# Kernel optimization log

Hardware: AMD Instinct MI355X
Metric: run time of the kernel (lower is better)

## Reference

```python
import jax, jax.numpy as jnp
import numpy as np

B, C_IN, C_OUT, C_KEY, N = 8, 512, 512, 256, 2048


def setup_inputs() -> dict:
    key = jax.random.key(0)
    k1, k2, k3, k4 = jax.random.split(key, 4)
    x = jax.random.normal(k1, (B, C_IN, N), dtype=jnp.float32)
    # Conv1d(kernel=1, bias=False) weights -> plain linear maps over channel dim
    Wq = jax.random.normal(k2, (C_KEY, C_IN), dtype=jnp.float32) * (1.0 / np.sqrt(C_IN))
    Wk = jax.random.normal(k3, (C_KEY, C_IN), dtype=jnp.float32) * (1.0 / np.sqrt(C_IN))
    Wv = jax.random.normal(k4, (C_OUT, C_IN), dtype=jnp.float32) * (1.0 / np.sqrt(C_IN))
    return {"x": x, "Wq": Wq, "Wk": Wk, "Wv": Wv}


def reference(x, Wq, Wk, Wv):
    # 1x1 conv projections: [B, C, N] -> [B, Ck/Co, N]
    q = jnp.einsum("oc,bcn->bon", Wq, x)
    k = jnp.einsum("oc,bcn->bon", Wk, x)
    v = jnpqv = jnp.einsum("oc,bcn->bon", Wv, x)
    # sim_map[b,i,j] = sum_c k[b,c,i] * q[b,c,j]  (unscaled)
    sim = jnp.einsum("bci,bcj->bij", k, q)  # [B, N, N]
    attn = jax.nn.softmax(sim, axis=-1)
    # out = value @ sim_map, then permute(0,2,1) -> [B, N, C_out]
    out = jnp.einsum("bck,bkm->bmc", jnpqv, attn)
    return out
```

## Files before the change

kernel.cpp:

```cpp
#include <hip/hip_runtime.h>

typedef _Float16 half8 __attribute__((ext_vector_type(8)));
typedef _Float16 half4v __attribute__((ext_vector_type(4)));
typedef _Float16 half2v __attribute__((ext_vector_type(2)));
typedef float f32x4 __attribute__((ext_vector_type(4)));

#define ASYNC_CP16(gp, lp)                                       \
  __builtin_amdgcn_global_load_lds(                              \
      (const __attribute__((address_space(1))) void*)(gp),       \
      (__attribute__((address_space(3))) void*)(lp), 16, 0, 0)

__global__ __launch_bounds__(256) void conv_w(const float* __restrict__ Wq,
                                              const float* __restrict__ Wk,
                                              const float* __restrict__ Wv,
                                              _Float16* __restrict__ Wb) {
  int idx = blockIdx.x * 256 + threadIdx.x;
  int row = idx >> 9;
  float v;
  if (row < 256)      v = Wq[idx];
  else if (row < 512) v = Wk[idx - 256 * 512];
  else                v = Wv[idx - 512 * 512];
  Wb[idx] = (_Float16)v;
}

__global__ __launch_bounds__(256) void conv_xT(const float* __restrict__ x,
                                               _Float16* __restrict__ xT) {
  __shared__ float T[32][33];
  const int b = blockIdx.z;
  const int n0 = blockIdx.x * 32, c0 = blockIdx.y * 32;
  const int t = threadIdx.x;
  const float* xb = x + (size_t)b * 512 * 2048;
  const int n2 = t & 15, cr = t >> 4;
#pragma unroll
  for (int r = 0; r < 2; r++) {
    int c = cr + r * 16;
    float2 v = *(const float2*)&xb[(size_t)(c0 + c) * 2048 + n0 + n2 * 2];
    T[c][n2 * 2] = v.x;
    T[c][n2 * 2 + 1] = v.y;
  }
  __syncthreads();
  _Float16* xtb = xT + (size_t)b * 2048 * 512;
  const int c2 = t & 15, nr = t >> 4;
#pragma unroll
  for (int r = 0; r < 2; r++) {
    int n = nr + r * 16;
    half2v h;
    h[0] = (_Float16)T[c2 * 2][n];
    h[1] = (_Float16)T[c2 * 2 + 1][n];
    *(half2v*)&xtb[(size_t)(n0 + n) * 512 + c0 + c2 * 2] = h;
  }
}

template <typename OutT, bool TR, bool STATS>
__global__ __launch_bounds__(256) void gemm_nt(const _Float16* __restrict__ A,
                                               const _Float16* __restrict__ B,
                                               OutT* __restrict__ C, int K,
                                               int lda, int ldb, int ldc,
                                               long sA, long sB, long sC,
                                               float* __restrict__ pm,
                                               float* __restrict__ ps) {
  A += (size_t)blockIdx.z * sA;
  B += (size_t)blockIdx.z * sB;
  C += (size_t)blockIdx.z * sC;
  const int m_blk = blockIdx.y * 128, n_blk = blockIdx.x * 128;

  __shared__ _Float16 As[2][4096];
  __shared__ _Float16 Bs[2][4096];

  const int t = threadIdx.x;
  const int lane = t & 63, wave = t >> 6;
  const int quad = lane >> 4, l16 = lane & 15;
  const int wm = (wave & 1) * 64, wn = (wave >> 1) * 64;

  const int srow = 16 * wave + (lane >> 2);
  const int schunk = (lane & 3) ^ ((lane >> 3) & 3);
  const _Float16* gA0 = A + (size_t)(m_blk + srow) * lda + schunk * 8;
  const _Float16* gA1 = gA0 + (size_t)64 * lda;
  const _Float16* gB0 = B + (size_t)(n_blk + srow) * ldb + schunk * 8;
  const _Float16* gB1 = gB0 + (size_t)64 * ldb;
  const int lofs = wave * 512 + lane * 8;

  const int rchunk = (quad ^ ((l16 >> 1) & 3)) * 8;

  f32x4 acc[4][4] = {};

  ASYNC_CP16(gA0, &As[0][lofs]);
  ASYNC_CP16(gA1, &As[0][lofs + 2048]);
  ASYNC_CP16(gB0, &Bs[0][lofs]);
  ASYNC_CP16(gB1, &Bs[0][lofs + 2048]);

  int ib = 0;
  for (int k0 = 0; k0 < K; k0 += 32, ib ^= 1) {
    __syncthreads();
    if (k0 + 32 < K) {
      ASYNC_CP16(gA0 + k0 + 32, &As[ib ^ 1][lofs]);
      ASYNC_CP16(gA1 + k0 + 32, &As[ib ^ 1][lofs + 2048]);
      ASYNC_CP16(gB0 + k0 + 32, &Bs[ib ^ 1][lofs]);
      ASYNC_CP16(gB1 + k0 + 32, &Bs[ib ^ 1][lofs + 2048]);
    }
    half8 af[4], bf[4];
#pragma unroll
    for (int i = 0; i < 4; i++) {
      af[i] = *(const half8*)&As[ib][(wm + i * 16 + l16) * 32 + rchunk];
      bf[i] = *(const half8*)&Bs[ib][(wn + i * 16 + l16) * 32 + rchunk];
    }
#pragma unroll
    for (int i = 0; i < 4; i++)
#pragma unroll
      for (int j = 0; j < 4; j++)
        acc[i][j] =
            __builtin_amdgcn_mfma_f32_16x16x32_f16(af[i], bf[j], acc[i][j], 0, 0, 0);
  }

#pragma unroll
  for (int i = 0; i < 4; i++) {
    const int m0 = m_blk + wm + i * 16 + quad * 4;
#pragma unroll
    for (int j = 0; j < 4; j++) {
      const int n0 = n_blk + wn + j * 16 + l16;
      if constexpr (TR) {
        if constexpr (sizeof(OutT) == 4) {
          *(f32x4*)&C[(size_t)n0 * ldc + m0] = acc[i][j];
        } else {
          half4v h;
          h[0] = (_Float16)acc[i][j][0];
          h[1] = (_Float16)acc[i][j][1];
          h[2] = (_Float16)acc[i][j][2];
          h[3] = (_Float16)acc[i][j][3];
          *(half4v*)&C[(size_t)n0 * ldc + m0] = h;
        }
      } else {
#pragma unroll
        for (int r = 0; r < 4; r++)
          C[(size_t)(m0 + r) * ldc + n0] = (OutT)acc[i][j][r];
      }
    }
  }

  if constexpr (STATS) {
    __shared__ float sred[2][128][2];
    const int wng = wave >> 1;
    float bmax[4][4], bsum[4][4];
#pragma unroll
    for (int i = 0; i < 4; i++) {
#pragma unroll
      for (int r = 0; r < 4; r++) {
        float mx = acc[i][0][r];
#pragma unroll
        for (int j = 1; j < 4; j++) mx = fmaxf(mx, acc[i][j][r]);
#pragma unroll
        for (int d = 1; d < 16; d <<= 1)
          mx = fmaxf(mx, __shfl_xor(mx, d, 64));
        float es = 0.f;
#pragma unroll
        for (int j = 0; j < 4; j++) es += __expf(acc[i][j][r] - mx);
#pragma unroll
        for (int d = 1; d < 16; d <<= 1) es += __shfl_xor(es, d, 64);
        bmax[i][r] = mx;
        bsum[i][r] = es;
      }
    }
    if (l16 == 0) {
#pragma unroll
      for (int i = 0; i < 4; i++)
#pragma unroll
        for (int r = 0; r < 4; r++) {
          int ml = wm + i * 16 + quad * 4 + r;
          sred[wng][ml][0] = bmax[i][r];
          sred[wng][ml][1] = bsum[i][r];
        }
    }
    __syncthreads();
    if (t < 128) {
      float m0 = sred[0][t][0], s0 = sred[0][t][1];
      float m1 = sred[1][t][0], s1 = sred[1][t][1];
      float M = fmaxf(m0, m1);
      float S = s0 * __expf(m0 - M) + s1 * __expf(m1 - M);
      size_t o = ((size_t)blockIdx.z * 16 + blockIdx.x) * 2048 + m_blk + t;
      pm[o] = M;
      ps[o] = S;
    }
  }
}

__global__ __launch_bounds__(256) void colstats2(const float* __restrict__ pm,
                                                 const float* __restrict__ ps,
                                                 float* __restrict__ shift) {
  const int idx = blockIdx.x * 256 + threadIdx.x;
  const int b = idx >> 11, col = idx & 2047;
  const float* pmb = pm + (size_t)b * 16 * 2048 + col;
  const float* psb = ps + (size_t)b * 16 * 2048 + col;
  float m = -3.0e38f;
#pragma unroll
  for (int i = 0; i < 16; i++) m = fmaxf(m, pmb[(size_t)i * 2048]);
  float s = 0.f;
#pragma unroll
  for (int i = 0; i < 16; i++)
    s += psb[(size_t)i * 2048] * __expf(pmb[(size_t)i * 2048] - m);
  shift[idx] = m + __logf(s);
}

__global__ __launch_bounds__(256) void attnscale(_Float16* __restrict__ simH,
                                                 const float* __restrict__ shift) {
  const size_t b = blockIdx.y;
  const size_t g = (size_t)blockIdx.x * 256 + threadIdx.x;
  const int col = (int)(g & 255) * 8;
  _Float16* p = simH + b * (2048ull * 2048) + g * 8;
  half8 h = *(const half8*)p;
  f32x4 s0 = *(const f32x4*)(shift + b * 2048 + col);
  f32x4 s1 = *(const f32x4*)(shift + b * 2048 + col + 4);
  half8 o;
#pragma unroll
  for (int i = 0; i < 4; i++) {
    o[i] = (_Float16)__expf((float)h[i] - s0[i]);
    o[i + 4] = (_Float16)__expf((float)h[i + 4] - s1[i]);
  }
  *(half8*)p = o;
}

extern "C" void kernel_launch(void* const* d_in, const int* in_sizes, int n_in,
                              void* d_out, int out_size, void* d_ws,
                              size_t ws_size, hipStream_t stream) {
  const float* x = (const float*)d_in[0];
  const float* Wq = (const float*)d_in[1];
  const float* Wk = (const float*)d_in[2];
  const float* Wv = (const float*)d_in[3];
  float* out = (float*)d_out;

  char* p = (char*)d_ws;
  auto alloc = [&](size_t bytes) -> char* {
    char* r = p;
    p += (bytes + 255) & ~(size_t)255;
    return r;
  };
  const size_t NB = 8, N = 2048, CIN = 512, CO = 512;
  _Float16* Wb = (_Float16*)alloc(1024 * 512 * sizeof(_Float16));
  _Float16* xT = (_Float16*)alloc(NB * N * CIN * sizeof(_Float16));
  _Float16* qkT = (_Float16*)alloc(NB * N * 512 * sizeof(_Float16));
  _Float16* v = (_Float16*)alloc(NB * CO * N * sizeof(_Float16));
  size_t base_used = (size_t)(p - (char*)d_ws);

  const size_t per_b =
      (size_t)N * N * 2 + 2 * 16 * N * 4 + N * 4 + 8192;
  int cb = 8;
  while (cb > 1 && base_used + (size_t)cb * per_b > ws_size) cb >>= 1;
  _Float16* simH = (_Float16*)alloc((size_t)cb * N * N * 2);
  float* pm = (float*)alloc((size_t)cb * 16 * N * 4);
  float* ps = (float*)alloc((size_t)cb * 16 * N * 4);
  float* shift = (float*)alloc((size_t)cb * N * 4);

  conv_w<<<dim3(1024 * 512 / 256), 256, 0, stream>>>(Wq, Wk, Wv, Wb);
  conv_xT<<<dim3(64, 16, 8), 256, 0, stream>>>(x, xT);

  gemm_nt<_Float16, true, false><<<dim3(16, 4, 8), 256, 0, stream>>>(
      Wb, xT, qkT, 512, 512, 512, 512, 0, (long)(N * CIN), (long)(N * 512),
      nullptr, nullptr);
  gemm_nt<_Float16, false, false><<<dim3(16, 4, 8), 256, 0, stream>>>(
      Wb + 512 * 512, xT, v, 512, 512, 512, 2048, 0, (long)(N * CIN),
      (long)(CO * N), nullptr, nullptr);

  for (int b0 = 0; b0 < 8; b0 += cb) {
    const _Float16* kT = qkT + (size_t)b0 * N * 512 + 256;
    const _Float16* qT = qkT + (size_t)b0 * N * 512;
    gemm_nt<_Float16, true, true><<<dim3(16, 16, cb), 256, 0, stream>>>(
        kT, qT, simH, 256, 512, 512, 2048, (long)(N * 512), (long)(N * 512),
        (long)(N * N), pm, ps);
    colstats2<<<dim3(cb * 8), 256, 0, stream>>>(pm, ps, shift);
    attnscale<<<dim3(2048, cb), 256, 0, stream>>>(simH, shift);
    gemm_nt<float, false, false><<<dim3(4, 16, cb), 256, 0, stream>>>(
        simH, v + (size_t)b0 * CO * N, out + (size_t)b0 * N * CO, 2048, 2048,
        2048, 512, (long)(N * N), (long)(CO * N), (long)(N * CO), nullptr,
        nullptr);
  }
}
```

Before: 241.2 us.

## Triple-buffer GEMM K-loop with partial vmcnt waits and fuse QK/V projections

Moves the shared GEMM kernel from double to triple buffering in LDS. Tiles are prefetched two steps ahead, and a raw s_waitcnt vmcnt(4) plus s_barrier replaces the full __syncthreads, so one tile's loads stay in flight while the current tile is computed. The separate QK and V projection launches become a single launch; blocks with m_blk at or above 512 write V in non-transposed layout into a second output pointer. The stats GEMM also rounds the accumulators to fp16 before the stats are computed, so the stats match the stored values. The cost is a larger LDS footprint, which may lower occupancy, and the hand-written wait count depends on assumptions about how the async loads are counted.

```diff
diff --git a/kernel.cpp b/kernel.cpp
--- a/kernel.cpp
+++ b/kernel.cpp
@@ -51,21 +51,20 @@
   }
 }
 
-template <typename OutT, bool TR, bool STATS>
-__global__ __launch_bounds__(256) void gemm_nt(const _Float16* __restrict__ A,
-                                               const _Float16* __restrict__ B,
-                                               OutT* __restrict__ C, int K,
-                                               int lda, int ldb, int ldc,
-                                               long sA, long sB, long sC,
-                                               float* __restrict__ pm,
-                                               float* __restrict__ ps) {
+template <typename OutT, bool TR, bool STATS, bool PROJ3>
+__global__ __launch_bounds__(256) void gemm_nt(
+    const _Float16* __restrict__ A, const _Float16* __restrict__ B,
+    OutT* __restrict__ C, OutT* __restrict__ C2, int K, int lda, int ldb,
+    int ldc, int ldc2, long sA, long sB, long sC, float* __restrict__ pm,
+    float* __restrict__ ps) {
   A += (size_t)blockIdx.z * sA;
   B += (size_t)blockIdx.z * sB;
   C += (size_t)blockIdx.z * sC;
+  if constexpr (PROJ3) C2 += (size_t)blockIdx.z * sC;
   const int m_blk = blockIdx.y * 128, n_blk = blockIdx.x * 128;
 
-  __shared__ _Float16 As[2][4096];
-  __shared__ _Float16 Bs[2][4096];
+  __shared__ _Float16 As[3][4096];
+  __shared__ _Float16 Bs[3][4096];
 
   const int t = threadIdx.x;
   const int lane = t & 63, wave = t >> 6;
@@ -88,15 +87,27 @@
   ASYNC_CP16(gA1, &As[0][lofs + 2048]);
   ASYNC_CP16(gB0, &Bs[0][lofs]);
   ASYNC_CP16(gB1, &Bs[0][lofs + 2048]);
+  if (32 < K) {
+    ASYNC_CP16(gA0 + 32, &As[1][lofs]);
+    ASYNC_CP16(gA1 + 32, &As[1][lofs + 2048]);
+    ASYNC_CP16(gB0 + 32, &Bs[1][lofs]);
+    ASYNC_CP16(gB1 + 32, &Bs[1][lofs + 2048]);
+  }
 
   int ib = 0;
-  for (int k0 = 0; k0 < K; k0 += 32, ib ^= 1) {
-    __syncthreads();
+  for (int k0 = 0; k0 < K; k0 += 32) {
     if (k0 + 32 < K) {
-      ASYNC_CP16(gA0 + k0 + 32, &As[ib ^ 1][lofs]);
-      ASYNC_CP16(gA1 + k0 + 32, &As[ib ^ 1][lofs + 2048]);
-      ASYNC_CP16(gB0 + k0 + 32, &Bs[ib ^ 1][lofs]);
-      ASYNC_CP16(gB1 + k0 + 32, &Bs[ib ^ 1][lofs + 2048]);
+      asm volatile("s_waitcnt vmcnt(4)\n\ts_barrier" ::: "memory");
+    } else {
+      asm volatile("s_waitcnt vmcnt(0)\n\ts_barrier" ::: "memory");
+    }
+    if (k0 + 64 < K) {
+      int nb = ib + 2;
+      if (nb >= 3) nb -= 3;
+      ASYNC_CP16(gA0 + k0 + 64, &As[nb][lofs]);
+      ASYNC_CP16(gA1 + k0 + 64, &As[nb][lofs + 2048]);
+      ASYNC_CP16(gB0 + k0 + 64, &Bs[nb][lofs]);
+      ASYNC_CP16(gB1 + k0 + 64, &Bs[nb][lofs + 2048]);
     }
     half8 af[4], bf[4];
 #pragma unroll
@@ -110,6 +121,8 @@
       for (int j = 0; j < 4; j++)
         acc[i][j] =
             __builtin_amdgcn_mfma_f32_16x16x32_f16(af[i], bf[j], acc[i][j], 0, 0, 0);
+    ib++;
+    if (ib == 3) ib = 0;
   }
 
 #pragma unroll
@@ -118,15 +131,28 @@
 #pragma unroll
     for (int j = 0; j < 4; j++) {
       const int n0 = n_blk + wn + j * 16 + l16;
-      if constexpr (TR) {
+      if constexpr (PROJ3) {
+        if (m_blk < 512) {
+          half4v h;
+#pragma unroll
+          for (int r = 0; r < 4; r++) h[r] = (_Float16)acc[i][j][r];
+          *(half4v*)&C[(size_t)n0 * ldc + m0] = h;
+        } else {
+#pragma unroll
+          for (int r = 0; r < 4; r++)
+            C2[(size_t)(m0 - 512 + r) * ldc2 + n0] = (OutT)acc[i][j][r];
+        }
+      } else if constexpr (TR) {
         if constexpr (sizeof(OutT) == 4) {
           *(f32x4*)&C[(size_t)n0 * ldc + m0] = acc[i][j];
         } else {
           half4v h;
-          h[0] = (_Float16)acc[i][j][0];
-          h[1] = (_Float16)acc[i][j][1];
-          h[2] = (_Float16)acc[i][j][2];
-          h[3] = (_Float16)acc[i][j][3];
+#pragma unroll
+          for (int r = 0; r < 4; r++) h[r] = (_Float16)acc[i][j][r];
+          if constexpr (STATS) {
+#pragma unroll
+            for (int r = 0; r < 4; r++) acc[i][j][r] = (float)h[r];
+          }
           *(half4v*)&C[(size_t)n0 * ldc + m0] = h;
         }
       } else {
@@ -252,24 +278,21 @@
   conv_w<<<dim3(1024 * 512 / 256), 256, 0, stream>>>(Wq, Wk, Wv, Wb);
   conv_xT<<<dim3(64, 16, 8), 256, 0, stream>>>(x, xT);
 
-  gemm_nt<_Float16, true, false><<<dim3(16, 4, 8), 256, 0, stream>>>(
-      Wb, xT, qkT, 512, 512, 512, 512, 0, (long)(N * CIN), (long)(N * 512),
-      nullptr, nullptr);
-  gemm_nt<_Float16, false, false><<<dim3(16, 4, 8), 256, 0, stream>>>(
-      Wb + 512 * 512, xT, v, 512, 512, 512, 2048, 0, (long)(N * CIN),
-      (long)(CO * N), nullptr, nullptr);
+  gemm_nt<_Float16, true, false, true><<<dim3(16, 8, 8), 256, 0, stream>>>(
+      Wb, xT, qkT, v, 512, 512, 512, 512, 2048, 0, (long)(N * CIN),
+      (long)(N * 512), nullptr, nullptr);
 
   for (int b0 = 0; b0 < 8; b0 += cb) {
     const _Float16* kT = qkT + (size_t)b0 * N * 512 + 256;
     const _Float16* qT = qkT + (size_t)b0 * N * 512;
-    gemm_nt<_Float16, true, true><<<dim3(16, 16, cb), 256, 0, stream>>>(
-        kT, qT, simH, 256, 512, 512, 2048, (long)(N * 512), (long)(N * 512),
-        (long)(N * N), pm, ps);
+    gemm_nt<_Float16, true, true, false><<<dim3(16, 16, cb), 256, 0, stream>>>(
+        kT, qT, simH, nullptr, 256, 512, 512, 2048, 0, (long)(N * 512),
+        (long)(N * 512), (long)(N * N), pm, ps);
     colstats2<<<dim3(cb * 8), 256, 0, stream>>>(pm, ps, shift);
     attnscale<<<dim3(2048, cb), 256, 0, stream>>>(simH, shift);
-    gemm_nt<float, false, false><<<dim3(4, 16, cb), 256, 0, stream>>>(
-        simH, v + (size_t)b0 * CO * N, out + (size_t)b0 * N * CO, 2048, 2048,
-        2048, 512, (long)(N * N), (long)(CO * N), (long)(N * CO), nullptr,
-        nullptr);
-  }
-}
+    gemm_nt<float, false, false, false><<<dim3(4, 16, cb), 256, 0, stream>>>(
+        simH, v + (size_t)b0 * CO * N, out + (size_t)b0 * N * CO, nullptr,
+        2048, 2048, 2048, 512, 0, (long)(N * N), (long)(CO * N),
+        (long)(N * CO), nullptr, nullptr);
+  }
+}
```

Result: no change. 239.2 us (-0.8%).
